# Optimization experiments

Measured on AMD Instinct MI355X. Metric: run time of the kernel, lower is better.

Reference implementation:

```python
import jax, jax.numpy as jnp
import numpy as np

N, E = 20000, 320000
EMB, HID, OUT, C, T = 300, 256, 128, 10, 3


def _glorot(k, shape):
    lim = np.sqrt(6.0 / (shape[0] + shape[1])).astype(np.float32)
    return jax.random.uniform(k, shape, jnp.float32, -lim, lim)


def setup_inputs() -> dict:
    key = jax.random.key(0)
    ks = jax.random.split(key, 32)
    inp = {}
    inp["x"] = jax.random.normal(ks[0], (N, EMB), jnp.float32)
    for t in range(T):
        inp[f"src{t}"] = jax.random.randint(ks[1 + t], (E,), 0, N, jnp.int32)
        inp[f"dst{t}"] = jax.random.randint(ks[4 + t], (E,), 0, N, jnp.int32)
    idx = 7
    for t in range(T):
        inp[f"W0_{t}"] = _glorot(ks[idx], (EMB, HID)); idx += 1
        inp[f"b0_{t}"] = jnp.zeros((HID,), jnp.float32)
        inp[f"W1_{t}"] = _glorot(ks[idx], (HID, OUT)); idx += 1
        inp[f"b1_{t}"] = jnp.zeros((OUT,), jnp.float32)
    inp["a0"] = _glorot(ks[idx], (1, 2 * HID))[0]; idx += 1
    inp["a1"] = _glorot(ks[idx], (1, 2 * OUT))[0]; idx += 1
    inp["fc_w"] = _glorot(ks[idx], (OUT, C)); idx += 1
    inp["fc_b"] = jnp.zeros((C,), jnp.float32)
    return inp


def _graph_conv(x, W, b, src, dst, n):
    # DGL GraphConv, norm='both': D_out^{-1/2} then sum-aggregate then D_in^{-1/2}
    h = x @ W  # weight applied first (in_feats > out_feats path); math identical
    ones = jnp.ones(src.shape[0], h.dtype)
    out_deg = jnp.clip(jax.ops.segment_sum(ones, src, num_segments=n), 1.0, None)
    in_deg = jnp.clip(jax.ops.segment_sum(ones, dst, num_segments=n), 1.0, None)
    h = h * jax.lax.rsqrt(out_deg)[:, None]
    agg = jax.ops.segment_sum(h[src], dst, num_segments=n)  # [n, F]
    return agg * jax.lax.rsqrt(in_deg)[:, None] + b


def _dual_attn_layer(x, Ws, bs, a, edges, n):
    hs = jnp.stack([_graph_conv(x, W, b, s, d, n)
                    for W, b, (s, d) in zip(Ws, bs, edges)], axis=0)  # [T, n, F]
    F = hs.shape[-1]
    mean_h = hs.mean(axis=0)  # [n, F]
    # (cat([h_i, mean_h]) * a).sum(-1) == h_i @ a[:F] + mean_h @ a[F:]
    sc = jnp.einsum('tnf,f->tn', hs, a[:F]) + mean_h @ a[F:]
    sc = jnp.where(sc > 0, sc, 0.2 * sc)  # LeakyReLU(0.2)
    attn = jax.nn.softmax(sc, axis=0)  # softmax over edge types
    return jnp.einsum('tn,tnf->nf', attn, hs)


def reference(x, src0, dst0, src1, dst1, src2, dst2,
              W0_0, b0_0, W1_0, b1_0, W0_1, b0_1, W1_1, b1_1,
              W0_2, b0_2, W1_2, b1_2, a0, a1, fc_w, fc_b):
    n = x.shape[0]
    edges = [(src0, dst0), (src1, dst1), (src2, dst2)]
    h = _dual_attn_layer(x, [W0_0, W0_1, W0_2], [b0_0, b0_1, b0_2], a0, edges, n)
    h = jnp.where(h > 0, h, 0.01 * h)  # torch.leaky_relu default slope; dropout=eval identity
    h = _dual_attn_layer(h, [W1_0, W1_1, W1_2], [b1_0, b1_1, b1_2], a1, edges, n)
    logits = h @ fc_w + fc_b
    return (h, logits)
```

## Files before the change

kernel.cpp:

```cpp
#include <hip/hip_runtime.h>
#include <hip/hip_fp16.h>

typedef unsigned short u16;
typedef unsigned int   u32;
typedef u16   u16x8  __attribute__((ext_vector_type(8)));
typedef u16   u16x4  __attribute__((ext_vector_type(4)));
typedef u16   u16x2  __attribute__((ext_vector_type(2)));
typedef short bf16x8 __attribute__((ext_vector_type(8)));
typedef float f32x4  __attribute__((ext_vector_type(4)));

#define GG 64
#define MAXN2 10016

__device__ inline u16 f2bf_rne(float f) {
    unsigned u = __float_as_uint(f);
    u += 0x7FFFu + ((u >> 16) & 1u);
    return (u16)(u >> 16);
}
__device__ inline float bf2f(u16 h) { return __uint_as_float(((unsigned)h) << 16); }
__device__ inline float h2f(u16 h) { return __half2float(__ushort_as_half(h)); }
__device__ inline u16 f2h(float f) { return __half_as_ushort(__float2half(f)); }

__global__ __launch_bounds__(256)
void hist_kernel(const int* __restrict__ s0, const int* __restrict__ d0,
                 const int* __restrict__ s1, const int* __restrict__ d1,
                 const int* __restrict__ s2, const int* __restrict__ d2,
                 u16* __restrict__ hist, int E, int Nn)
{
    const int b = blockIdx.x, side = blockIdx.y, z = blockIdx.z;
    const int* arr;
    if (side == 0) arr = (z == 0) ? s0 : ((z == 1) ? s1 : s2);
    else           arr = (z == 0) ? d0 : ((z == 1) ? d1 : d2);

    __shared__ u32 cnt[MAXN2];
    const int tid = threadIdx.x;
    const int half = Nn >> 1;
    for (int i = tid; i < half; i += 256) cnt[i] = 0;
    __syncthreads();

    const int chunk = (E + GG - 1) / GG;
    const int beg = b * chunk;
    const int end = min(E, beg + chunk);
    for (int e = beg + tid; e < end; e += 256) {
        const int nd = arr[e];
        atomicAdd(&cnt[nd >> 1], 1u << ((nd & 1) * 16));
    }
    __syncthreads();

    u32* row = (u32*)(hist + ((size_t)(z * 2 + side) * GG + b) * Nn);
    for (int i = tid; i < half; i += 256) row[i] = cnt[i];
}

__global__ __launch_bounds__(256)
void sumdeg_scales_kernel(const u16* __restrict__ hist,
                          int* __restrict__ deg, float* __restrict__ scales, int Nn)
{
    int id = blockIdx.x * 256 + threadIdx.x;
    if (id >= 6 * Nn) return;
    const int zs = id / Nn, node = id - zs * Nn;
    const u16* base = hist + (size_t)zs * GG * Nn + node;
    int sum = 0;
    #pragma unroll 8
    for (int b = 0; b < GG; ++b) sum += base[(size_t)b * Nn];
    const int side = zs & 1, z = zs >> 1;
    const int di = (side == 0 ? z : 3 + z) * Nn + node;
    deg[di] = sum;
    scales[di] = rsqrtf((float)max(sum, 1));
}

__global__ __launch_bounds__(1024)
void scan_rowptr_kernel(const int* __restrict__ deg,
                        int* __restrict__ rowptr,
                        int Nn)
{
    const int z = blockIdx.x;
    const int* d = deg + (size_t)(3 + z) * Nn;
    int* rp = rowptr + (size_t)z * (Nn + 1);
    const int t = threadIdx.x;
    const int chunk = (Nn + 1023) / 1024;
    const int beg = t * chunk;
    const int end = min(beg + chunk, Nn);

    int partial = 0;
    for (int i = beg; i < end; ++i) partial += d[i];

    __shared__ int s[1024];
    s[t] = partial;
    __syncthreads();
    #pragma unroll
    for (int off = 1; off < 1024; off <<= 1) {
        int v = (t >= off) ? s[t - off] : 0;
        __syncthreads();
        s[t] += v;
        __syncthreads();
    }
    const int excl = s[t] - partial;

    int run = excl;
    for (int i = beg; i < end; ++i) { rp[i] = run; run += d[i]; }
    if (t == 1023) rp[Nn] = s[1023];
}

__global__ __launch_bounds__(256)
void offsets_kernel(const u16* __restrict__ hist, const int* __restrict__ rowptr,
                    u32* __restrict__ offu, int Nn)
{
    int id = blockIdx.x * 256 + threadIdx.x;
    if (id >= 3 * Nn) return;
    const int z = id / Nn, node = id - z * Nn;
    const u16* hbase = hist + ((size_t)(z * 2 + 1) * GG) * Nn + node;
    u32* obase = offu + (size_t)z * GG * Nn + node;
    u32 run = (u32)rowptr[(size_t)z * (Nn + 1) + node];
    for (int b = 0; b < GG; ++b) {
        const u32 c = hbase[(size_t)b * Nn];
        obase[(size_t)b * Nn] = run;
        run += c;
    }
}

__global__ __launch_bounds__(256)
void fill_csr_kernel(const int* __restrict__ s0, const int* __restrict__ d0,
                     const int* __restrict__ s1, const int* __restrict__ d1,
                     const int* __restrict__ s2, const int* __restrict__ d2,
                     const u32* __restrict__ offu,
                     int* __restrict__ csr, int E, int Nn)
{
    const int b = blockIdx.x, z = blockIdx.z;
    const int* sp = (z == 0) ? s0 : ((z == 1) ? s1 : s2);
    const int* dp = (z == 0) ? d0 : ((z == 1) ? d1 : d2);

    __shared__ u32 cur[MAXN2];
    const int tid = threadIdx.x;
    const int half = Nn >> 1;
    for (int i = tid; i < half; i += 256) cur[i] = 0;
    __syncthreads();

    const u32* orow = offu + ((size_t)z * GG + b) * Nn;
    int* crow = csr + (size_t)z * E;
    const int chunk = (E + GG - 1) / GG;
    const int beg = b * chunk;
    const int end = min(E, beg + chunk);
    for (int e = beg + tid; e < end; e += 256) {
        const int d = dp[e];
        const int s = sp[e];
        const u32 old = atomicAdd(&cur[d >> 1], 1u << ((d & 1) * 16));
        const u32 rank = (old >> ((d & 1) * 16)) & 0xFFFFu;
        crow[orow[d] + rank] = s;
    }
}

__global__ __launch_bounds__(256)
void wtransp3_kernel(const float* __restrict__ Wa, const float* __restrict__ Wb,
                     const float* __restrict__ Wc,
                     u16* __restrict__ Th, u16* __restrict__ Tl,
                     int K, int N, int Kpad)
{
    const int z = blockIdx.z;
    const float* W = (z == 0) ? Wa : ((z == 1) ? Wb : Wc);
    u16* th = Th + (size_t)z * N * Kpad;
    u16* tl = Tl + (size_t)z * N * Kpad;
    int id = blockIdx.x * 256 + threadIdx.x;
    if (id >= N * Kpad) return;
    int n = id / Kpad, kp = id - n * Kpad;
    float v = (kp < K) ? W[(size_t)kp * N + n] : 0.f;
    u16 hi = f2bf_rne(v);
    u16 lo = f2bf_rne(v - bf2f(hi));
    th[id] = hi; tl[id] = lo;
}

__global__ __launch_bounds__(256)
void aconv_kernel(const float* __restrict__ X, u16* __restrict__ Xh, u16* __restrict__ Xl,
                  int Mreal, int K, int Kpad, int total)
{
    int id = blockIdx.x * 256 + threadIdx.x;
    if (id >= total) return;
    int r = id / Kpad, kp = id - r * Kpad;
    float v = (r < Mreal && kp < K) ? X[(size_t)r * K + kp] : 0.f;
    u16 hi = f2bf_rne(v);
    u16 lo = f2bf_rne(v - bf2f(hi));
    Xh[id] = hi; Xl[id] = lo;
}

template<int KSTEPS>
__global__ __launch_bounds__(256)
void mfma_gemm_kernel(const u16* __restrict__ Ah, const u16* __restrict__ Al,
                      const u16* __restrict__ B0h, const u16* __restrict__ B0l,
                      const u16* __restrict__ B1h, const u16* __restrict__ B1l,
                      const u16* __restrict__ B2h, const u16* __restrict__ B2l,
                      const float* __restrict__ scales,
                      u16* __restrict__ Cbase, int M, int Ncols)
{
    const int z = blockIdx.z;
    const u16* Bh = (z == 0) ? B0h : ((z == 1) ? B1h : B2h);
    const u16* Bl = (z == 0) ? B0l : ((z == 1) ? B1l : B2l);
    const float* s = scales + (size_t)z * M;
    u16* C = Cbase + (size_t)z * M * Ncols;
    const int Kpad = KSTEPS * 32;

    __shared__ u16 Ash[128 * 32], Asl[128 * 32], Bsh[128 * 32], Bsl[128 * 32];

    const int tid  = threadIdx.x;
    const int lane = tid & 63;
    const int wv   = tid >> 6;
    const int wr   = wv >> 1, wc = wv & 1;
    const int g    = lane >> 4, lm = lane & 15;
    const int row0 = blockIdx.y * 128, col0 = blockIdx.x * 128;

    const int sr = tid >> 1;
    const int sh = tid & 1;
    const int swz = (sr >> 1) & 3;
    const int c0 = ((sh * 2 + 0) ^ swz) << 4;
    const int c1 = ((sh * 2 + 1) ^ swz) << 4;
    const size_t abase = (size_t)(row0 + sr) * Kpad;
    const size_t bbase = (size_t)(col0 + sr) * Kpad;

    f32x4 acc[4][4];
    #pragma unroll
    for (int i = 0; i < 4; ++i)
        #pragma unroll
        for (int j = 0; j < 4; ++j) acc[i][j] = 0.f;

    int kg = sh * 16;
    u16x8 ah0 = *(const u16x8*)(Ah + abase + kg);
    u16x8 ah1 = *(const u16x8*)(Ah + abase + kg + 8);
    u16x8 al0 = *(const u16x8*)(Al + abase + kg);
    u16x8 al1 = *(const u16x8*)(Al + abase + kg + 8);
    u16x8 bh0 = *(const u16x8*)(Bh + bbase + kg);
    u16x8 bh1 = *(const u16x8*)(Bh + bbase + kg + 8);
    u16x8 bl0 = *(const u16x8*)(Bl + bbase + kg);
    u16x8 bl1 = *(const u16x8*)(Bl + bbase + kg + 8);

    for (int st = 0; st < KSTEPS; ++st) {
        {
            char* pAh = (char*)Ash + sr * 64;
            char* pAl = (char*)Asl + sr * 64;
            char* pBh = (char*)Bsh + sr * 64;
            char* pBl = (char*)Bsl + sr * 64;
            *(u16x8*)(pAh + c0) = ah0;
            *(u16x8*)(pAh + c1) = ah1;
            *(u16x8*)(pAl + c0) = al0;
            *(u16x8*)(pAl + c1) = al1;
            *(u16x8*)(pBh + c0) = bh0;
            *(u16x8*)(pBh + c1) = bh1;
            *(u16x8*)(pBl + c0) = bl0;
            *(u16x8*)(pBl + c1) = bl1;
        }
        __syncthreads();

        if (st + 1 < KSTEPS) {
            const int kgn = (st + 1) * 32 + sh * 16;
            ah0 = *(const u16x8*)(Ah + abase + kgn);
            ah1 = *(const u16x8*)(Ah + abase + kgn + 8);
            al0 = *(const u16x8*)(Al + abase + kgn);
            al1 = *(const u16x8*)(Al + abase + kgn + 8);
            bh0 = *(const u16x8*)(Bh + bbase + kgn);
            bh1 = *(const u16x8*)(Bh + bbase + kgn + 8);
            bl0 = *(const u16x8*)(Bl + bbase + kgn);
            bl1 = *(const u16x8*)(Bl + bbase + kgn + 8);
        }

        bf16x8 afh[4], afl[4], bfh[4], bfl[4];
        #pragma unroll
        for (int mi = 0; mi < 4; ++mi) {
            const int r = wr * 64 + mi * 16 + lm;
            const int byte = r * 64 + ((g ^ ((r >> 1) & 3)) << 4);
            afh[mi] = *(const bf16x8*)((const char*)Ash + byte);
            afl[mi] = *(const bf16x8*)((const char*)Asl + byte);
        }
        #pragma unroll
        for (int ni = 0; ni < 4; ++ni) {
            const int r = wc * 64 + ni * 16 + lm;
            const int byte = r * 64 + ((g ^ ((r >> 1) & 3)) << 4);
            bfh[ni] = *(const bf16x8*)((const char*)Bsh + byte);
            bfl[ni] = *(const bf16x8*)((const char*)Bsl + byte);
        }
        #pragma unroll
        for (int mi = 0; mi < 4; ++mi)
            #pragma unroll
            for (int ni = 0; ni < 4; ++ni) {
                acc[mi][ni] = __builtin_amdgcn_mfma_f32_16x16x32_bf16(afl[mi], bfh[ni], acc[mi][ni], 0, 0, 0);
                acc[mi][ni] = __builtin_amdgcn_mfma_f32_16x16x32_bf16(afh[mi], bfl[ni], acc[mi][ni], 0, 0, 0);
                acc[mi][ni] = __builtin_amdgcn_mfma_f32_16x16x32_bf16(afh[mi], bfh[ni], acc[mi][ni], 0, 0, 0);
            }

        __syncthreads();
    }

    #pragma unroll
    for (int mi = 0; mi < 4; ++mi) {
        #pragma unroll
        for (int reg = 0; reg < 4; ++reg) {
            const int r = row0 + wr * 64 + mi * 16 + g * 4 + reg;
            if (r < M) {
                const float sc = s[r];
                #pragma unroll
                for (int ni = 0; ni < 4; ++ni) {
                    C[(size_t)r * Ncols + col0 + wc * 64 + ni * 16 + lm] = f2h(acc[mi][ni][reg] * sc);
                }
            }
        }
    }
}

template <int F, int VEC, bool LEAKY01, bool FUSE_FC, bool OUT_SPLIT>
__global__ __launch_bounds__(256)
void gather_attn_kernel(const u16* __restrict__ pre,
                        const int* __restrict__ rowptr,
                        const int* __restrict__ csr,
                        const float* __restrict__ sin_,
                        const float* __restrict__ bb0, const float* __restrict__ bb1,
                        const float* __restrict__ bb2,
                        const float* __restrict__ a,
                        const float* __restrict__ fcw,
                        const float* __restrict__ fcb,
                        float* __restrict__ out,
                        u16* __restrict__ outh, u16* __restrict__ outl,
                        float* __restrict__ logits,
                        int Nn, int E)
{
    const int wave = blockIdx.x * 4 + (threadIdx.x >> 6);
    const int lane = threadIdx.x & 63;
    if (wave >= Nn) return;
    const int n = wave;
    const size_t NF = (size_t)Nn * F;
    const int fo = lane * VEC;

    float ht[3][VEC];
    float mean[VEC];
    #pragma unroll
    for (int v = 0; v < VEC; ++v) mean[v] = 0.f;

    const float* bptr[3] = {bb0, bb1, bb2};
    #pragma unroll
    for (int t = 0; t < 3; ++t) {
        const int* rp = rowptr + (size_t)t * (Nn + 1);
        const int beg = rp[n];
        const int end = rp[n + 1];
        const int* lst = csr + (size_t)t * E;
        const u16* P = pre + t * NF;

        float a0v[VEC], a1v[VEC], a2v[VEC], a3v[VEC];
        #pragma unroll
        for (int v = 0; v < VEC; ++v) { a0v[v] = 0.f; a1v[v] = 0.f; a2v[v] = 0.f; a3v[v] = 0.f; }

        for (int j = beg; j < end; j += 64) {
            const int cnt = min(64, end - j);
            int myIdx = (lane < cnt) ? lst[j + lane] : 0;
            int k = 0;
            for (; k + 4 <= cnt; k += 4) {
                const int s0 = __shfl(myIdx, k + 0);
                const int s1 = __shfl(myIdx, k + 1);
                const int s2 = __shfl(myIdx, k + 2);
                const int s3 = __shfl(myIdx, k + 3);
                if constexpr (VEC == 4) {
                    u16x4 r0 = *reinterpret_cast<const u16x4*>(P + (size_t)s0 * F + fo);
                    u16x4 r1 = *reinterpret_cast<const u16x4*>(P + (size_t)s1 * F + fo);
                    u16x4 r2 = *reinterpret_cast<const u16x4*>(P + (size_t)s2 * F + fo);
                    u16x4 r3 = *reinterpret_cast<const u16x4*>(P + (size_t)s3 * F + fo);
                    #pragma unroll
                    for (int v = 0; v < 4; ++v) a0v[v] += h2f(r0[v]);
                    #pragma unroll
                    for (int v = 0; v < 4; ++v) a1v[v] += h2f(r1[v]);
                    #pragma unroll
                    for (int v = 0; v < 4; ++v) a2v[v] += h2f(r2[v]);
                    #pragma unroll
                    for (int v = 0; v < 4; ++v) a3v[v] += h2f(r3[v]);
                } else {
                    u16x2 r0 = *reinterpret_cast<const u16x2*>(P + (size_t)s0 * F + fo);
                    u16x2 r1 = *reinterpret_cast<const u16x2*>(P + (size_t)s1 * F + fo);
                    u16x2 r2 = *reinterpret_cast<const u16x2*>(P + (size_t)s2 * F + fo);
                    u16x2 r3 = *reinterpret_cast<const u16x2*>(P + (size_t)s3 * F + fo);
                    a0v[0] += h2f(r0[0]); a0v[1] += h2f(r0[1]);
                    a1v[0] += h2f(r1[0]); a1v[1] += h2f(r1[1]);
                    a2v[0] += h2f(r2[0]); a2v[1] += h2f(r2[1]);
                    a3v[0] += h2f(r3[0]); a3v[1] += h2f(r3[1]);
                }
            }
            for (; k < cnt; ++k) {
                const int sI = __shfl(myIdx, k);
                const u16* rowp = P + (size_t)sI * F + fo;
                if constexpr (VEC == 4) {
                    u16x4 r4 = *reinterpret_cast<const u16x4*>(rowp);
                    #pragma unroll
                    for (int v = 0; v < 4; ++v) a0v[v] += h2f(r4[v]);
                } else {
                    u16x2 r2 = *reinterpret_cast<const u16x2*>(rowp);
                    a0v[0] += h2f(r2[0]); a0v[1] += h2f(r2[1]);
                }
            }
        }

        const float si = sin_[t * Nn + n];
        const float* bp = bptr[t] + fo;
        #pragma unroll
        for (int v = 0; v < VEC; ++v) {
            const float sum = (a0v[v] + a1v[v]) + (a2v[v] + a3v[v]);
            const float xv = fmaf(sum, si, bp[v]);
            ht[t][v] = xv;
            mean[v] += xv;
        }
    }
    #pragma unroll
    for (int v = 0; v < VEC; ++v) mean[v] *= (1.0f / 3.0f);

    float p0 = 0.f, p1 = 0.f, p2 = 0.f, p3 = 0.f;
    #pragma unroll
    for (int v = 0; v < VEC; ++v) {
        const float aA = a[fo + v];
        const float aB = a[F + fo + v];
        p0 = fmaf(ht[0][v], aA, p0);
        p1 = fmaf(ht[1][v], aA, p1);
        p2 = fmaf(ht[2][v], aA, p2);
        p3 = fmaf(mean[v], aB, p3);
    }
    #pragma unroll
    for (int off = 1; off < 64; off <<= 1) {
        p0 += __shfl_xor(p0, off);
        p1 += __shfl_xor(p1, off);
        p2 += __shfl_xor(p2, off);
        p3 += __shfl_xor(p3, off);
    }
    float sc0 = p0 + p3, sc1 = p1 + p3, sc2 = p2 + p3;
    sc0 = sc0 > 0.f ? sc0 : 0.2f * sc0;
    sc1 = sc1 > 0.f ? sc1 : 0.2f * sc1;
    sc2 = sc2 > 0.f ? sc2 : 0.2f * sc2;
    const float m = fmaxf(sc0, fmaxf(sc1, sc2));
    const float e0 = __expf(sc0 - m);
    const float e1 = __expf(sc1 - m);
    const float e2 = __expf(sc2 - m);
    const float inv = 1.0f / (e0 + e1 + e2);
    const float at0 = e0 * inv, at1 = e1 * inv, at2 = e2 * inv;

    float o[VEC];
    #pragma unroll
    for (int v = 0; v < VEC; ++v) {
        float ov = at0 * ht[0][v] + at1 * ht[1][v] + at2 * ht[2][v];
        if constexpr (LEAKY01) ov = ov > 0.f ? ov : 0.01f * ov;
        o[v] = ov;
    }

    if constexpr (OUT_SPLIT) {
        u16 oh[VEC], ol[VEC];
        #pragma unroll
        for (int v = 0; v < VEC; ++v) {
            u16 hi = f2bf_rne(o[v]);
            oh[v] = hi;
            ol[v] = f2bf_rne(o[v] - bf2f(hi));
        }
        if constexpr (VEC == 4) {
            *(u16x4*)(outh + (size_t)n * F + fo) = *(u16x4*)oh;
            *(u16x4*)(outl + (size_t)n * F + fo) = *(u16x4*)ol;
        } else {
            *(u16x2*)(outh + (size_t)n * F + fo) = *(u16x2*)oh;
            *(u16x2*)(outl + (size_t)n * F + fo) = *(u16x2*)ol;
        }
    } else {
        float* op = out + (size_t)n * F + fo;
        #pragma unroll
        for (int v = 0; v < VEC; ++v) op[v] = o[v];
    }

    if constexpr (FUSE_FC) {
        float accc[10];
        #pragma unroll
        for (int c = 0; c < 10; ++c) {
            float s = 0.f;
            #pragma unroll
            for (int v = 0; v < VEC; ++v)
                s = fmaf(o[v], fcw[(fo + v) * 10 + c], s);
            accc[c] = s;
        }
        #pragma unroll
        for (int off = 1; off < 64; off <<= 1) {
            #pragma unroll
            for (int c = 0; c < 10; ++c) accc[c] += __shfl_xor(accc[c], off);
        }
        if (lane == 0) {
            #pragma unroll
            for (int c = 0; c < 10; ++c)
                logits[(size_t)n * 10 + c] = accc[c] + fcb[c];
        }
    }
}

extern "C" void kernel_launch(void* const* d_in, const int* in_sizes, int n_in,
                              void* d_out, int out_size, void* d_ws, size_t ws_size,
                              hipStream_t stream)
{
    const float* x = (const float*)d_in[0];
    const int* src[3] = {(const int*)d_in[1], (const int*)d_in[3], (const int*)d_in[5]};
    const int* dst[3] = {(const int*)d_in[2], (const int*)d_in[4], (const int*)d_in[6]};
    const float* W0[3] = {(const float*)d_in[7],  (const float*)d_in[11], (const float*)d_in[15]};
    const float* b0[3] = {(const float*)d_in[8],  (const float*)d_in[12], (const float*)d_in[16]};
    const float* W1[3] = {(const float*)d_in[9],  (const float*)d_in[13], (const float*)d_in[17]};
    const float* b1[3] = {(const float*)d_in[10], (const float*)d_in[14], (const float*)d_in[18]};
    const float* a0  = (const float*)d_in[19];
    const float* a1  = (const float*)d_in[20];
    const float* fcw = (const float*)d_in[21];
    const float* fcb = (const float*)d_in[22];

    const int Nn = in_sizes[0] / 300;
    const int E  = in_sizes[1];
    const int K1 = 300, K1p = 320, F1 = 256;
    const int K2p = 256, F2 = 128;
    const int Mpad = ((Nn + 127) / 128) * 128;

    char* wsb = (char*)d_ws;
    size_t off = 0;
    auto take = [&](size_t bytes) { char* p = wsb + off; off = (off + bytes + 15) & ~(size_t)15; return p; };
    int*   deg    = (int*)take(6 * (size_t)Nn * sizeof(int));
    float* scales = (float*)take(6 * (size_t)Nn * sizeof(float));
    int*   rowptr = (int*)take(3 * ((size_t)Nn + 1) * sizeof(int));
    int*   csr    = (int*)take(3 * (size_t)E * sizeof(int));
    u16*   wt1h   = (u16*)take(3 * (size_t)F1 * K1p * sizeof(u16));
    u16*   wt1l   = (u16*)take(3 * (size_t)F1 * K1p * sizeof(u16));
    u16*   wt2h   = (u16*)take(3 * (size_t)F2 * K2p * sizeof(u16));
    u16*   wt2l   = (u16*)take(3 * (size_t)F2 * K2p * sizeof(u16));
    const size_t histB = 6 * (size_t)GG * Nn * sizeof(u16);
    const size_t offuB = 3 * (size_t)GG * Nn * sizeof(u32);
    const size_t gemmB = (3 * (size_t)Nn * 256 + 2 * (size_t)Mpad * K1p + 2 * (size_t)Mpad * K2p) * sizeof(u16);
    char* region = (char*)take(histB + offuB > gemmB ? histB + offuB : gemmB);
    u16* hist = (u16*)region;
    u32* offu = (u32*)(region + ((histB + 15) & ~(size_t)15));
    u16* buf1 = (u16*)region;
    u16* xh   = buf1 + 3 * (size_t)Nn * 256;
    u16* xl   = xh + (size_t)Mpad * K1p;
    u16* h1h  = xl + (size_t)Mpad * K1p;
    u16* h1l  = h1h + (size_t)Mpad * K2p;

    float* outH   = (float*)d_out;
    float* logits = outH + (size_t)Nn * 128;

    {
        dim3 g(GG, 2, 3);
        hist_kernel<<<g, 256, 0, stream>>>(src[0], dst[0], src[1], dst[1],
                                           src[2], dst[2], hist, E, Nn);
    }
    sumdeg_scales_kernel<<<(6 * Nn + 255) / 256, 256, 0, stream>>>(hist, deg, scales, Nn);
    scan_rowptr_kernel<<<3, 1024, 0, stream>>>(deg, rowptr, Nn);
    offsets_kernel<<<(3 * Nn + 255) / 256, 256, 0, stream>>>(hist, rowptr, offu, Nn);
    {
        dim3 g(GG, 1, 3);
        fill_csr_kernel<<<g, 256, 0, stream>>>(src[0], dst[0], src[1], dst[1],
                                               src[2], dst[2], offu, csr, E, Nn);
    }

    {
        dim3 g1((F1 * K1p + 255) / 256, 1, 3);
        wtransp3_kernel<<<g1, 256, 0, stream>>>(W0[0], W0[1], W0[2], wt1h, wt1l, K1, F1, K1p);
        dim3 g2((F2 * K2p + 255) / 256, 1, 3);
        wtransp3_kernel<<<g2, 256, 0, stream>>>(W1[0], W1[1], W1[2], wt2h, wt2l, 256, F2, K2p);
    }
    {
        const int total = Mpad * K1p;
        aconv_kernel<<<(total + 255) / 256, 256, 0, stream>>>(x, xh, xl, Nn, K1, K1p, total);
    }

    {
        dim3 g(F1 / 128, Mpad / 128, 3);
        mfma_gemm_kernel<10><<<g, 256, 0, stream>>>(
            xh, xl,
            wt1h + 0 * (size_t)F1 * K1p, wt1l + 0 * (size_t)F1 * K1p,
            wt1h + 1 * (size_t)F1 * K1p, wt1l + 1 * (size_t)F1 * K1p,
            wt1h + 2 * (size_t)F1 * K1p, wt1l + 2 * (size_t)F1 * K1p,
            scales, buf1, Nn, F1);
    }
    gather_attn_kernel<256, 4, true, false, true><<<(Nn + 3) / 4, 256, 0, stream>>>(
        buf1, rowptr, csr, scales + 3 * (size_t)Nn,
        b0[0], b0[1], b0[2], a0, nullptr, nullptr,
        nullptr, h1h, h1l, nullptr, Nn, E);

    {
        dim3 g(F2 / 128, Mpad / 128, 3);
        mfma_gemm_kernel<8><<<g, 256, 0, stream>>>(
            h1h, h1l,
            wt2h + 0 * (size_t)F2 * K2p, wt2l + 0 * (size_t)F2 * K2p,
            wt2h + 1 * (size_t)F2 * K2p, wt2l + 1 * (size_t)F2 * K2p,
            wt2h + 2 * (size_t)F2 * K2p, wt2l + 2 * (size_t)F2 * K2p,
            scales, buf1, Nn, F2);
    }
    gather_attn_kernel<128, 2, false, true, false><<<(Nn + 3) / 4, 256, 0, stream>>>(
        buf1, rowptr, csr, scales + 3 * (size_t)Nn,
        b1[0], b1[1], b1[2], a1, fcw, fcb,
        outH, nullptr, nullptr, logits, Nn, E);
}
```

Before: 306.9 us.

## Fuse conversion kernels, merge CSR fill into first GEMM launch, shrink histogram groups

Merges the three weight/input bf16 split-conversion launches into one kernel. The CSR fill becomes extra blocks of the first GEMM launch so the two independent jobs share a single launch. The histogram group count drops from 64 to 16, which shrinks the histogram and offset arrays and the per-node reduction loops. The trade-off is fewer, longer blocks for hist and fill, and GEMM blocks that now reserve a larger shared buffer. Workspace buffers no longer alias each other, so they need more memory.

```diff
diff --git a/kernel.cpp b/kernel.cpp
--- a/kernel.cpp
+++ b/kernel.cpp
@@ -9,7 +9,7 @@
 typedef short bf16x8 __attribute__((ext_vector_type(8)));
 typedef float f32x4  __attribute__((ext_vector_type(4)));
 
-#define GG 64
+#define GG 16
 #define MAXN2 10016
 
 __device__ inline u16 f2bf_rne(float f) {
@@ -60,7 +60,7 @@
     const int zs = id / Nn, node = id - zs * Nn;
     const u16* base = hist + (size_t)zs * GG * Nn + node;
     int sum = 0;
-    #pragma unroll 8
+    #pragma unroll
     for (int b = 0; b < GG; ++b) sum += base[(size_t)b * Nn];
     const int side = zs & 1, z = zs >> 1;
     const int di = (side == 0 ? z : 3 + z) * Nn + node;
@@ -111,6 +111,7 @@
     const u16* hbase = hist + ((size_t)(z * 2 + 1) * GG) * Nn + node;
     u32* obase = offu + (size_t)z * GG * Nn + node;
     u32 run = (u32)rowptr[(size_t)z * (Nn + 1) + node];
+    #pragma unroll
     for (int b = 0; b < GG; ++b) {
         const u32 c = hbase[(size_t)b * Nn];
         obase[(size_t)b * Nn] = run;
@@ -119,92 +120,108 @@
 }
 
 __global__ __launch_bounds__(256)
-void fill_csr_kernel(const int* __restrict__ s0, const int* __restrict__ d0,
-                     const int* __restrict__ s1, const int* __restrict__ d1,
-                     const int* __restrict__ s2, const int* __restrict__ d2,
-                     const u32* __restrict__ offu,
-                     int* __restrict__ csr, int E, int Nn)
-{
-    const int b = blockIdx.x, z = blockIdx.z;
-    const int* sp = (z == 0) ? s0 : ((z == 1) ? s1 : s2);
-    const int* dp = (z == 0) ? d0 : ((z == 1) ? d1 : d2);
-
-    __shared__ u32 cur[MAXN2];
-    const int tid = threadIdx.x;
-    const int half = Nn >> 1;
-    for (int i = tid; i < half; i += 256) cur[i] = 0;
-    __syncthreads();
-
-    const u32* orow = offu + ((size_t)z * GG + b) * Nn;
-    int* crow = csr + (size_t)z * E;
-    const int chunk = (E + GG - 1) / GG;
-    const int beg = b * chunk;
-    const int end = min(E, beg + chunk);
-    for (int e = beg + tid; e < end; e += 256) {
-        const int d = dp[e];
-        const int s = sp[e];
-        const u32 old = atomicAdd(&cur[d >> 1], 1u << ((d & 1) * 16));
-        const u32 rank = (old >> ((d & 1) * 16)) & 0xFFFFu;
-        crow[orow[d] + rank] = s;
-    }
-}
-
-__global__ __launch_bounds__(256)
-void wtransp3_kernel(const float* __restrict__ Wa, const float* __restrict__ Wb,
-                     const float* __restrict__ Wc,
-                     u16* __restrict__ Th, u16* __restrict__ Tl,
-                     int K, int N, int Kpad)
-{
-    const int z = blockIdx.z;
-    const float* W = (z == 0) ? Wa : ((z == 1) ? Wb : Wc);
-    u16* th = Th + (size_t)z * N * Kpad;
-    u16* tl = Tl + (size_t)z * N * Kpad;
+void convert_all_kernel(const float* __restrict__ x,
+                        const float* __restrict__ W0a, const float* __restrict__ W0b,
+                        const float* __restrict__ W0c,
+                        const float* __restrict__ W1a, const float* __restrict__ W1b,
+                        const float* __restrict__ W1c,
+                        u16* __restrict__ wt1h, u16* __restrict__ wt1l,
+                        u16* __restrict__ wt2h, u16* __restrict__ wt2l,
+                        u16* __restrict__ xh, u16* __restrict__ xl,
+                        int Nn, int n1, int n2, int n3)
+{
     int id = blockIdx.x * 256 + threadIdx.x;
-    if (id >= N * Kpad) return;
-    int n = id / Kpad, kp = id - n * Kpad;
-    float v = (kp < K) ? W[(size_t)kp * N + n] : 0.f;
-    u16 hi = f2bf_rne(v);
-    u16 lo = f2bf_rne(v - bf2f(hi));
-    th[id] = hi; tl[id] = lo;
-}
-
-__global__ __launch_bounds__(256)
-void aconv_kernel(const float* __restrict__ X, u16* __restrict__ Xh, u16* __restrict__ Xl,
-                  int Mreal, int K, int Kpad, int total)
-{
-    int id = blockIdx.x * 256 + threadIdx.x;
-    if (id >= total) return;
-    int r = id / Kpad, kp = id - r * Kpad;
-    float v = (r < Mreal && kp < K) ? X[(size_t)r * K + kp] : 0.f;
-    u16 hi = f2bf_rne(v);
-    u16 lo = f2bf_rne(v - bf2f(hi));
-    Xh[id] = hi; Xl[id] = lo;
+    float v;
+    u16 *th, *tl;
+    int outi;
+    if (id < n1) {
+        const int per = 256 * 320;
+        const int z = id / per, rem = id - z * per;
+        const int n = rem / 320, kp = rem - n * 320;
+        const float* W = (z == 0) ? W0a : ((z == 1) ? W0b : W0c);
+        v = (kp < 300) ? W[kp * 256 + n] : 0.f;
+        th = wt1h; tl = wt1l; outi = id;
+    } else if (id < n1 + n2) {
+        const int id2 = id - n1;
+        const int per = 128 * 256;
+        const int z = id2 / per, rem = id2 - z * per;
+        const int n = rem / 256, kp = rem - n * 256;
+        const float* W = (z == 0) ? W1a : ((z == 1) ? W1b : W1c);
+        v = W[kp * 128 + n];
+        th = wt2h; tl = wt2l; outi = id2;
+    } else if (id < n1 + n2 + n3) {
+        const int id3 = id - n1 - n2;
+        const int r = id3 / 320, kp = id3 - r * 320;
+        v = (r < Nn && kp < 300) ? x[(size_t)r * 300 + kp] : 0.f;
+        th = xh; tl = xl; outi = id3;
+    } else return;
+    const u16 hi = f2bf_rne(v);
+    th[outi] = hi;
+    tl[outi] = f2bf_rne(v - bf2f(hi));
 }
 
 template<int KSTEPS>
 __global__ __launch_bounds__(256)
-void mfma_gemm_kernel(const u16* __restrict__ Ah, const u16* __restrict__ Al,
+void gemm_fill_kernel(const u16* __restrict__ Ah, const u16* __restrict__ Al,
                       const u16* __restrict__ B0h, const u16* __restrict__ B0l,
                       const u16* __restrict__ B1h, const u16* __restrict__ B1l,
                       const u16* __restrict__ B2h, const u16* __restrict__ B2l,
                       const float* __restrict__ scales,
-                      u16* __restrict__ Cbase, int M, int Ncols)
-{
-    const int z = blockIdx.z;
+                      u16* __restrict__ Cbase, int M, int Ncols,
+                      int NBX, int NBY,
+                      const int* __restrict__ s0, const int* __restrict__ d0,
+                      const int* __restrict__ s1, const int* __restrict__ d1,
+                      const int* __restrict__ s2, const int* __restrict__ d2,
+                      const u32* __restrict__ offu, int* __restrict__ csr,
+                      int E, int nFill)
+{
+    __shared__ u32 smem[MAXN2];
+    const int tid = threadIdx.x;
+
+    if ((int)blockIdx.x < nFill) {
+        const int fb = blockIdx.x;
+        const int z = fb / GG, b = fb - z * GG;
+        const int* sp = (z == 0) ? s0 : ((z == 1) ? s1 : s2);
+        const int* dp = (z == 0) ? d0 : ((z == 1) ? d1 : d2);
+        const int half = M >> 1;
+        for (int i = tid; i < half; i += 256) smem[i] = 0;
+        __syncthreads();
+        const u32* orow = offu + ((size_t)z * GG + b) * M;
+        int* crow = csr + (size_t)z * E;
+        const int chunk = (E + GG - 1) / GG;
+        const int beg = b * chunk;
+        const int end = min(E, beg + chunk);
+        for (int e = beg + tid; e < end; e += 256) {
+            const int d = dp[e];
+            const int s = sp[e];
+            const u32 old = atomicAdd(&smem[d >> 1], 1u << ((d & 1) * 16));
+            const u32 rank = (old >> ((d & 1) * 16)) & 0xFFFFu;
+            crow[orow[d] + rank] = s;
+        }
+        return;
+    }
+
+    const int g2 = blockIdx.x - nFill;
+    const int bx = g2 % NBX;
+    const int by = (g2 / NBX) % NBY;
+    const int z = g2 / (NBX * NBY);
+
+    u16* Ash = (u16*)smem;
+    u16* Asl = (u16*)smem + 4096;
+    u16* Bsh = (u16*)smem + 8192;
+    u16* Bsl = (u16*)smem + 12288;
+
     const u16* Bh = (z == 0) ? B0h : ((z == 1) ? B1h : B2h);
     const u16* Bl = (z == 0) ? B0l : ((z == 1) ? B1l : B2l);
     const float* s = scales + (size_t)z * M;
     u16* C = Cbase + (size_t)z * M * Ncols;
     const int Kpad = KSTEPS * 32;
 
-    __shared__ u16 Ash[128 * 32], Asl[128 * 32], Bsh[128 * 32], Bsl[128 * 32];
-
-    const int tid  = threadIdx.x;
     const int lane = tid & 63;
     const int wv   = tid >> 6;
     const int wr   = wv >> 1, wc = wv & 1;
     const int g    = lane >> 4, lm = lane & 15;
-    const int row0 = blockIdx.y * 128, col0 = blockIdx.x * 128;
+    const int row0 = by * 128, col0 = bx * 128;
 
     const int sr = tid >> 1;
     const int sh = tid & 1;
@@ -220,7 +237,7 @@
         #pragma unroll
         for (int j = 0; j < 4; ++j) acc[i][j] = 0.f;
 
-    int kg = sh * 16;
+    const int kg = sh * 16;
     u16x8 ah0 = *(const u16x8*)(Ah + abase + kg);
     u16x8 ah1 = *(const u16x8*)(Ah + abase + kg + 8);
     u16x8 al0 = *(const u16x8*)(Al + abase + kg);
@@ -501,7 +518,7 @@
 
     const int Nn = in_sizes[0] / 300;
     const int E  = in_sizes[1];
-    const int K1 = 300, K1p = 320, F1 = 256;
+    const int K1p = 320, F1 = 256;
     const int K2p = 256, F2 = 128;
     const int Mpad = ((Nn + 127) / 128) * 128;
 
@@ -512,21 +529,17 @@
     float* scales = (float*)take(6 * (size_t)Nn * sizeof(float));
     int*   rowptr = (int*)take(3 * ((size_t)Nn + 1) * sizeof(int));
     int*   csr    = (int*)take(3 * (size_t)E * sizeof(int));
+    u16*   hist   = (u16*)take(6 * (size_t)GG * Nn * sizeof(u16));
+    u32*   offu   = (u32*)take(3 * (size_t)GG * Nn * sizeof(u32));
     u16*   wt1h   = (u16*)take(3 * (size_t)F1 * K1p * sizeof(u16));
     u16*   wt1l   = (u16*)take(3 * (size_t)F1 * K1p * sizeof(u16));
     u16*   wt2h   = (u16*)take(3 * (size_t)F2 * K2p * sizeof(u16));
     u16*   wt2l   = (u16*)take(3 * (size_t)F2 * K2p * sizeof(u16));
-    const size_t histB = 6 * (size_t)GG * Nn * sizeof(u16);
-    const size_t offuB = 3 * (size_t)GG * Nn * sizeof(u32);
-    const size_t gemmB = (3 * (size_t)Nn * 256 + 2 * (size_t)Mpad * K1p + 2 * (size_t)Mpad * K2p) * sizeof(u16);
-    char* region = (char*)take(histB + offuB > gemmB ? histB + offuB : gemmB);
-    u16* hist = (u16*)region;
-    u32* offu = (u32*)(region + ((histB + 15) & ~(size_t)15));
-    u16* buf1 = (u16*)region;
-    u16* xh   = buf1 + 3 * (size_t)Nn * 256;
-    u16* xl   = xh + (size_t)Mpad * K1p;
-    u16* h1h  = xl + (size_t)Mpad * K1p;
-    u16* h1l  = h1h + (size_t)Mpad * K2p;
+    u16*   buf1   = (u16*)take(3 * (size_t)Nn * 256 * sizeof(u16));
+    u16*   xh     = (u16*)take((size_t)Mpad * K1p * sizeof(u16));
+    u16*   xl     = (u16*)take((size_t)Mpad * K1p * sizeof(u16));
+    u16*   h1h    = (u16*)take((size_t)Mpad * K2p * sizeof(u16));
+    u16*   h1l    = (u16*)take((size_t)Mpad * K2p * sizeof(u16));
 
     float* outH   = (float*)d_out;
     float* logits = outH + (size_t)Nn * 128;
@@ -536,34 +549,31 @@
         hist_kernel<<<g, 256, 0, stream>>>(src[0], dst[0], src[1], dst[1],
                                            src[2], dst[2], hist, E, Nn);
     }
+    {
+        const int n1 = 3 * F1 * K1p;
+        const int n2 = 3 * F2 * K2p;
+        const int n3 = Mpad * K1p;
+        const int total = n1 + n2 + n3;
+        convert_all_kernel<<<(total + 255) / 256, 256, 0, stream>>>(
+            x, W0[0], W0[1], W0[2], W1[0], W1[1], W1[2],
+            wt1h, wt1l, wt2h, wt2l, xh, xl, Nn, n1, n2, n3);
+    }
     sumdeg_scales_kernel<<<(6 * Nn + 255) / 256, 256, 0, stream>>>(hist, deg, scales, Nn);
     scan_rowptr_kernel<<<3, 1024, 0, stream>>>(deg, rowptr, Nn);
     offsets_kernel<<<(3 * Nn + 255) / 256, 256, 0, stream>>>(hist, rowptr, offu, Nn);
+
     {
-        dim3 g(GG, 1, 3);
-        fill_csr_kernel<<<g, 256, 0, stream>>>(src[0], dst[0], src[1], dst[1],
-                                               src[2], dst[2], offu, csr, E, Nn);
-    }
-
-    {
-        dim3 g1((F1 * K1p + 255) / 256, 1, 3);
-        wtransp3_kernel<<<g1, 256, 0, stream>>>(W0[0], W0[1], W0[2], wt1h, wt1l, K1, F1, K1p);
-        dim3 g2((F2 * K2p + 255) / 256, 1, 3);
-        wtransp3_kernel<<<g2, 256, 0, stream>>>(W1[0], W1[1], W1[2], wt2h, wt2l, 256, F2, K2p);
-    }
-    {
-        const int total = Mpad * K1p;
-        aconv_kernel<<<(total + 255) / 256, 256, 0, stream>>>(x, xh, xl, Nn, K1, K1p, total);
-    }
-
-    {
-        dim3 g(F1 / 128, Mpad / 128, 3);
-        mfma_gemm_kernel<10><<<g, 256, 0, stream>>>(
+        const int NBX = F1 / 128, NBY = Mpad / 128;
+        const int nFill = 3 * GG;
+        const int total = nFill + NBX * NBY * 3;
+        gemm_fill_kernel<10><<<total, 256, 0, stream>>>(
             xh, xl,
             wt1h + 0 * (size_t)F1 * K1p, wt1l + 0 * (size_t)F1 * K1p,
             wt1h + 1 * (size_t)F1 * K1p, wt1l + 1 * (size_t)F1 * K1p,
             wt1h + 2 * (size_t)F1 * K1p, wt1l + 2 * (size_t)F1 * K1p,
-            scales, buf1, Nn, F1);
+            scales, buf1, Nn, F1, NBX, NBY,
+            src[0], dst[0], src[1], dst[1], src[2], dst[2],
+            offu, csr, E, nFill);
     }
     gather_attn_kernel<256, 4, true, false, true><<<(Nn + 3) / 4, 256, 0, stream>>>(
         buf1, rowptr, csr, scales + 3 * (size_t)Nn,
@@ -571,13 +581,16 @@
         nullptr, h1h, h1l, nullptr, Nn, E);
 
     {
-        dim3 g(F2 / 128, Mpad / 128, 3);
-        mfma_gemm_kernel<8><<<g, 256, 0, stream>>>(
+        const int NBX = F2 / 128, NBY = Mpad / 128;
+        const int total = NBX * NBY * 3;
+        gemm_fill_kernel<8><<<total, 256, 0, stream>>>(
             h1h, h1l,
             wt2h + 0 * (size_t)F2 * K2p, wt2l + 0 * (size_t)F2 * K2p,
             wt2h + 1 * (size_t)F2 * K2p, wt2l + 1 * (size_t)F2 * K2p,
             wt2h + 2 * (size_t)F2 * K2p, wt2l + 2 * (size_t)F2 * K2p,
-            scales, buf1, Nn, F2);
+            scales, buf1, Nn, F2, NBX, NBY,
+            src[0], dst[0], src[1], dst[1], src[2], dst[2],
+            offu, csr, E, 0);
     }
     gather_attn_kernel<128, 2, false, true, false><<<(Nn + 3) / 4, 256, 0, stream>>>(
         buf1, rowptr, csr, scales + 3 * (size_t)Nn,
```

Result: slower. 314.4 us (+2.4%).
